# Optimization experiments

Measured on AMD Instinct MI355X. Metric: run time of the kernel, lower is better.

Reference implementation:

```python
import jax, jax.numpy as jnp
import numpy as np

B, LQ, LK, E, HID, H = 4, 1024, 2048, 512, 512, 8


def _ln(x, g, b, eps=1e-5):
    mu = jnp.mean(x, -1, keepdims=True)
    var = jnp.mean((x - mu) ** 2, -1, keepdims=True)
    return (x - mu) * jax.lax.rsqrt(var + eps) * g + b


def _mha(q_in, k_in, v_in, Wq, bq, Wk, bk, Wv, bv, Wo, bo, nheads, q_valid, k_valid):
    # torch nn.MultiheadAttention (batch_first, eval/dropout=0) math
    Bq, Lq, Em = q_in.shape
    Lk = k_in.shape[1]
    hd = Em // nheads
    q = (q_in @ Wq.T + bq).reshape(Bq, Lq, nheads, hd)
    k = (k_in @ Wk.T + bk).reshape(Bq, Lk, nheads, hd)
    v = (v_in @ Wv.T + bv).reshape(Bq, Lk, nheads, hd)
    scale = 1.0 / np.sqrt(hd).astype(np.float32)
    s = jnp.einsum('bqhd,bkhd->bhqk', q, k) * scale
    if k_valid is not None:
        # valid query rows may only attend to valid key columns
        s = jnp.where(k_valid[:, None, None, :], s, jnp.finfo(s.dtype).min)
    w = jax.nn.softmax(s, axis=-1)
    # rows beyond a sample's length are fully masked in the torch nested path
    # (softmax -> NaN, later nan_to_num'd to 0); we zero them directly.
    w = jnp.where(q_valid[:, None, :, None], w, 0.0)
    o = jnp.einsum('bhqk,bkhd->bqhd', w, v).reshape(Bq, Lq, Em)
    return o @ Wo.T + bo, jnp.mean(w, axis=1)  # weights averaged over heads


def setup_inputs() -> dict:
    key = jax.random.key(0)
    ks = jax.random.split(key, 32)
    p = lambda i, shape: 0.02 * jax.random.normal(ks[i], shape, dtype=jnp.float32)
    inp = {
        'queries': jax.random.normal(ks[0], (B, LQ, E), dtype=jnp.float32),
        'keys': jax.random.normal(ks[1], (B, LK, E), dtype=jnp.float32),
        'q_len': jax.random.randint(ks[2], (B,), 1, LQ + 1),
        # cross-attention params
        'cWq': p(3, (E, E)), 'cbq': jnp.zeros((E,)),
        'cWk': p(4, (E, E)), 'cbk': jnp.zeros((E,)),
        'cWv': p(5, (E, E)), 'cbv': jnp.zeros((E,)),
        'cWo': p(6, (E, E)), 'cbo': jnp.zeros((E,)),
        # self-attention params
        'sWq': p(7, (HID, HID)), 'sbq': jnp.zeros((HID,)),
        'sWk': p(8, (HID, HID)), 'sbk': jnp.zeros((HID,)),
        'sWv': p(9, (HID, HID)), 'sbv': jnp.zeros((HID,)),
        'sWo': p(10, (HID, HID)), 'sbo': jnp.zeros((HID,)),
        # ffn + norms
        'Wf': p(11, (HID, E)), 'bf': jnp.zeros((HID,)),
        'g_cross': jnp.ones((E,)), 'b_cross': jnp.zeros((E,)),
        'g_ffn': jnp.ones((HID,)), 'b_ffn': jnp.zeros((HID,)),
        'g_self': jnp.ones((HID,)), 'b_self': jnp.zeros((HID,)),
    }
    return inp


def reference(queries, keys, q_len,
              cWq, cbq, cWk, cbk, cWv, cbv, cWo, cbo,
              sWq, sbq, sWk, sbk, sWv, sbv, sWo, sbo,
              Wf, bf, g_cross, b_cross, g_ffn, b_ffn, g_self, b_self):
    valid = jnp.arange(LQ)[None, :] < q_len[:, None]  # [B, LQ] ragged lengths
    q = jnp.where(valid[..., None], queries, 0.0)     # nested -> padded with 0
    # cross attention: valid rows attend to ALL keys (per the nested mask)
    cross, weights = _mha(q, keys, keys, cWq, cbq, cWk, cbk, cWv, cbv, cWo, cbo,
                          H, valid, None)
    q = _ln(jax.nn.silu(cross + q), g_cross, b_cross)
    f = q @ Wf.T + bf
    q = _ln(jax.nn.silu(q + f), g_ffn, b_ffn)  # q_dim == hidden_dim branch
    q = jnp.where(valid[..., None], q, 0.0)    # torch.nan_to_num on padded rows
    # self attention: valid rows attend only to valid rows of the same sample
    so, _ = _mha(q, q, q, sWq, sbq, sWk, sbk, sWv, sbv, sWo, sbo, H, valid, valid)
    q = _ln(jax.nn.silu(q + so), g_self, b_self)
    q = jnp.where(valid[..., None], q, 0.0)    # padded rows discarded by unbind
    return q, weights
```

## Files before the change

kernel.cpp:

```cpp
#include <hip/hip_runtime.h>

#define BB 4
#define SLQ 1024
#define SLK 2048
#define EE 512
#define HH 8
#define HD 64

typedef unsigned short u16;
typedef __attribute__((ext_vector_type(8))) short s16x8;
typedef __attribute__((ext_vector_type(4))) float f32x4;

__device__ __forceinline__ float bf2f(u16 u) {
  union { unsigned int i; float f; } v; v.i = ((unsigned int)u) << 16; return v.f;
}
__device__ __forceinline__ u16 f2bf(float f) {
  union { float f; unsigned int i; } v; v.f = f;
  unsigned int i = v.i;
  return (u16)((i + 0x7fffu + ((i >> 16) & 1u)) >> 16);
}

__device__ __forceinline__ void async16(const u16* g, u16* l) {
  __builtin_amdgcn_global_load_lds(
      (const __attribute__((address_space(1))) unsigned int*)g,
      (__attribute__((address_space(3))) unsigned int*)l, 16, 0, 0);
}

template<int BM, int BN, int MODE, int SKIPQ>
__global__ __launch_bounds__(256, (BM == 128 ? 4 : 6))
void gemm_nt(const u16* __restrict__ A, const u16* __restrict__ Bm,
             const float* __restrict__ bias, u16* __restrict__ C,
             int M, int N, int K, int lda, int ldb, int ldc,
             long sAz, long sBz, long sCz, float alpha, int Lsub,
             const int* __restrict__ qlen)
{
  constexpr int WTM = BM / 2, WTN = BN / 2;
  constexpr int MI = WTM / 16, NI = WTN / 16;
  constexpr int EPAD = WTN + 8;
  constexpr int SM1 = (BM + BN) * 32;
  constexpr int SM2 = (MODE == 0) ? 4 * WTM * EPAD : 0;
  constexpr int SM = (SM1 > SM2) ? SM1 : SM2;

  const int z = blockIdx.z;
  const int tileM = blockIdx.y * BM;
  const int tileN = blockIdx.x * BN;

  if (SKIPQ == 1) { if (tileM >= qlen[z >> 3]) return; }
  if (SKIPQ == 2) { int b = tileM >> 10; if ((tileM & 1023) >= qlen[b]) return; }

  __shared__ __align__(16) u16 smem[SM];
  u16* ldsA = smem;
  u16* ldsB = smem + BM * 32;

  const int t = threadIdx.x;
  const int lane = t & 63;
  const int wave = t >> 6;
  const int waveM = wave >> 1;
  const int waveN = wave & 1;
  const int lm = lane & 15;
  const int kg = lane >> 4;

  const u16* Ab = A + (long)z * sAz + (long)tileM * lda;
  const u16* Bb = Bm + (long)z * sBz + (long)tileN * ldb;

  f32x4 acc[MI][NI];
#pragma unroll
  for (int i = 0; i < MI; ++i)
#pragma unroll
    for (int j = 0; j < NI; ++j) acc[i][j] = (f32x4){0.f, 0.f, 0.f, 0.f};

  for (int kt = 0; kt < K; kt += 32) {
    __syncthreads();
#pragma unroll
    for (int i = 0; i < (BM * 4) / 256; ++i) {
      int c = i * 256 + t;
      async16(Ab + (long)(c >> 2) * lda + kt + (c & 3) * 8, ldsA + (c - lane) * 8);
    }
#pragma unroll
    for (int i = 0; i < (BN * 4) / 256; ++i) {
      int c = i * 256 + t;
      async16(Bb + (long)(c >> 2) * ldb + kt + (c & 3) * 8, ldsB + (c - lane) * 8);
    }
    __syncthreads();

    s16x8 aF[MI], bF[NI];
#pragma unroll
    for (int i = 0; i < MI; ++i)
      aF[i] = *(const s16x8*)&ldsA[(waveM * WTM + i * 16 + lm) * 32 + kg * 8];
#pragma unroll
    for (int j = 0; j < NI; ++j)
      bF[j] = *(const s16x8*)&ldsB[(waveN * WTN + j * 16 + lm) * 32 + kg * 8];
#pragma unroll
    for (int i = 0; i < MI; ++i)
#pragma unroll
      for (int j = 0; j < NI; ++j)
        acc[i][j] = __builtin_amdgcn_mfma_f32_16x16x32_bf16(aF[i], bF[j], acc[i][j], 0, 0, 0);
  }

  if (MODE == 0) {
    u16* ep = smem + wave * (WTM * EPAD);
    __syncthreads();
#pragma unroll
    for (int i = 0; i < MI; ++i)
#pragma unroll
      for (int j = 0; j < NI; ++j) {
        int n = waveN * WTN + j * 16 + lm;
        float bv = bias ? bias[tileN + n] : 0.0f;
#pragma unroll
        for (int r = 0; r < 4; ++r)
          ep[(i * 16 + kg * 4 + r) * EPAD + j * 16 + lm] = f2bf(acc[i][j][r] * alpha + bv);
      }
    const long Crow = (long)z * sCz + (long)(tileM + waveM * WTM) * ldc + tileN + waveN * WTN;
#pragma unroll
    for (int it = 0; it < (WTM * WTN) / 512; ++it) {
      int idx = it * 64 + lane;
      int row = idx / (WTN / 8), seg = idx % (WTN / 8);
      *(uint4*)&C[Crow + (long)row * ldc + seg * 8] =
          *(const uint4*)&ep[row * EPAD + seg * 8];
    }
  } else {
#pragma unroll
    for (int j = 0; j < NI; ++j) {
      int n = tileN + waveN * WTN + j * 16 + lm;
      float bv = bias ? bias[n] : 0.0f;
#pragma unroll
      for (int i = 0; i < MI; ++i) {
#pragma unroll
        for (int r = 0; r < 4; ++r) {
          int m = tileM + waveM * WTM + i * 16 + kg * 4 + r;
          float v = acc[i][j][r] * alpha + bv;
          int b = m / Lsub, l = m - b * Lsub;
          int h = n >> 6, d = n & 63;
          C[(((long)(b * HH + h) * Lsub + l) << 6) + d] = f2bf(v);
        }
      }
    }
  }
}

template<int BM, int BN, int SKIPQ, int NPROJ>
__global__ __launch_bounds__(256, 6)
void gemm_proj(const u16* __restrict__ A,
               const u16* B0, const u16* B1, const u16* B2,
               const float* bias0, const float* bias1, const float* bias2,
               u16* C0, u16* C1, u16* C2,
               int M, int lda, int Lsub, const int* __restrict__ qlen)
{
  constexpr int WTM = BM / 2, WTN = BN / 2;
  constexpr int MI = WTM / 16, NI = WTN / 16;

  const int z = blockIdx.z;
  const int tileM = blockIdx.y * BM;
  const int tileN = blockIdx.x * BN;
  if (SKIPQ == 2) { int b = tileM >> 10; if ((tileM & 1023) >= qlen[b]) return; }

  const u16* Bm = (z == 0) ? B0 : (z == 1) ? B1 : B2;
  const float* bias = (z == 0) ? bias0 : (z == 1) ? bias1 : bias2;
  u16* C = (z == 0) ? C0 : (z == 1) ? C1 : C2;
  const bool tr = (z == NPROJ - 1);

  __shared__ __align__(16) u16 smem[(BM + BN) * 32];
  u16* ldsA = smem;
  u16* ldsB = smem + BM * 32;

  const int t = threadIdx.x;
  const int lane = t & 63;
  const int wave = t >> 6;
  const int waveM = wave >> 1;
  const int waveN = wave & 1;
  const int lm = lane & 15;
  const int kg = lane >> 4;

  const u16* Ab = A + (long)tileM * lda;
  const u16* Bb = Bm + (long)tileN * EE;

  f32x4 acc[MI][NI];
#pragma unroll
  for (int i = 0; i < MI; ++i)
#pragma unroll
    for (int j = 0; j < NI; ++j) acc[i][j] = (f32x4){0.f, 0.f, 0.f, 0.f};

  for (int kt = 0; kt < EE; kt += 32) {
    __syncthreads();
#pragma unroll
    for (int i = 0; i < (BM * 4) / 256; ++i) {
      int c = i * 256 + t;
      async16(Ab + (long)(c >> 2) * lda + kt + (c & 3) * 8, ldsA + (c - lane) * 8);
    }
#pragma unroll
    for (int i = 0; i < (BN * 4) / 256; ++i) {
      int c = i * 256 + t;
      async16(Bb + (long)(c >> 2) * EE + kt + (c & 3) * 8, ldsB + (c - lane) * 8);
    }
    __syncthreads();

    s16x8 aF[MI], bF[NI];
#pragma unroll
    for (int i = 0; i < MI; ++i)
      aF[i] = *(const s16x8*)&ldsA[(waveM * WTM + i * 16 + lm) * 32 + kg * 8];
#pragma unroll
    for (int j = 0; j < NI; ++j)
      bF[j] = *(const s16x8*)&ldsB[(waveN * WTN + j * 16 + lm) * 32 + kg * 8];
#pragma unroll
    for (int i = 0; i < MI; ++i)
#pragma unroll
      for (int j = 0; j < NI; ++j)
        acc[i][j] = __builtin_amdgcn_mfma_f32_16x16x32_bf16(aF[i], bF[j], acc[i][j], 0, 0, 0);
  }

  if (!tr) {
#pragma unroll
    for (int j = 0; j < NI; ++j) {
      int n = tileN + waveN * WTN + j * 16 + lm;
      float bv = bias[n];
#pragma unroll
      for (int i = 0; i < MI; ++i)
#pragma unroll
        for (int r = 0; r < 4; ++r) {
          int m = tileM + waveM * WTM + i * 16 + kg * 4 + r;
          int b = m / Lsub, l = m - b * Lsub;
          int h = n >> 6, d = n & 63;
          C[(((long)(b * HH + h) * Lsub + l) << 6) + d] = f2bf(acc[i][j][r] + bv);
        }
    }
  } else {
    constexpr int PAD = BM + 8;
    const int bb = tileM / Lsub;
    const int l0 = tileM - bb * Lsub;
#pragma unroll
    for (int c = 0; c < BN / 32; ++c) {
      __syncthreads();
#pragma unroll
      for (int j = 0; j < NI; ++j) {
        int nloc = waveN * WTN + j * 16 + lm;
        if (nloc >= c * 32 && nloc < c * 32 + 32) {
          int nl = nloc - c * 32;
          float bv = bias[tileN + nloc];
#pragma unroll
          for (int i = 0; i < MI; ++i)
#pragma unroll
            for (int r = 0; r < 4; ++r) {
              int mm = waveM * WTM + i * 16 + kg * 4 + r;
              smem[nl * PAD + mm] = f2bf(acc[i][j][r] + bv);
            }
        }
      }
      __syncthreads();
#pragma unroll
      for (int v = 0; v < (32 * BM) / (256 * 8); ++v) {
        int idx = v * 256 + t;
        int nl = idx / (BM / 8), m8 = idx % (BM / 8);
        int n = tileN + c * 32 + nl;
        int h = n >> 6, d = n & 63;
        *(uint4*)&C[((long)(bb * HH + h) * HD + d) * Lsub + l0 + m8 * 8] =
            *(const uint4*)&smem[nl * PAD + m8 * 8];
      }
    }
  }
}

__global__ __launch_bounds__(256)
void softmax_stats_wmean(const u16* __restrict__ S, float* __restrict__ outw,
                         float2* __restrict__ stats, const int* __restrict__ qlen) {
  int row = blockIdx.x;
  int b = row >> 10, q = row & 1023;
  int t = threadIdx.x, lane = t & 63, w = t >> 6;
  float* wr = outw + (long)row * SLK;
  if (q >= qlen[b]) {
    float4 z = {0.f, 0.f, 0.f, 0.f};
    *(float4*)(wr + t * 8) = z; *(float4*)(wr + t * 8 + 4) = z;
    return;
  }
  __shared__ float acc4[4][2048];
#pragma unroll
  for (int hh = 0; hh < 2; ++hh) {
    int h = 2 * w + hh;
    const u16* p = S + ((long)((b * HH + h) * SLQ + q)) * SLK;
    float x[4][8];
    float m = -1e30f;
#pragma unroll
    for (int c = 0; c < 4; ++c) {
      s16x8 v = *(const s16x8*)(p + c * 512 + lane * 8);
#pragma unroll
      for (int j = 0; j < 8; ++j) { x[c][j] = bf2f((u16)v[j]); m = fmaxf(m, x[c][j]); }
    }
#pragma unroll
    for (int o = 1; o <= 32; o <<= 1) m = fmaxf(m, __shfl_xor(m, o));
    float s = 0.f;
#pragma unroll
    for (int c = 0; c < 4; ++c)
#pragma unroll
      for (int j = 0; j < 8; ++j) { x[c][j] = __expf(x[c][j] - m); s += x[c][j]; }
#pragma unroll
    for (int o = 1; o <= 32; o <<= 1) s += __shfl_xor(s, o);
    if (lane == 0) stats[(long)(b * HH + h) * SLQ + q] = (float2){m, s};
    float sc = 0.125f / s;
#pragma unroll
    for (int c = 0; c < 4; ++c) {
      float4 v0 = {x[c][0] * sc, x[c][1] * sc, x[c][2] * sc, x[c][3] * sc};
      float4 v1 = {x[c][4] * sc, x[c][5] * sc, x[c][6] * sc, x[c][7] * sc};
      if (hh == 0) {
        *(float4*)&acc4[w][c * 512 + lane * 8] = v0;
        *(float4*)&acc4[w][c * 512 + lane * 8 + 4] = v1;
      } else {
        float4 a0 = *(const float4*)&acc4[w][c * 512 + lane * 8];
        float4 a1 = *(const float4*)&acc4[w][c * 512 + lane * 8 + 4];
        a0.x += v0.x; a0.y += v0.y; a0.z += v0.z; a0.w += v0.w;
        a1.x += v1.x; a1.y += v1.y; a1.z += v1.z; a1.w += v1.w;
        *(float4*)&acc4[w][c * 512 + lane * 8] = a0;
        *(float4*)&acc4[w][c * 512 + lane * 8 + 4] = a1;
      }
    }
  }
  __syncthreads();
#pragma unroll
  for (int u = 0; u < 2; ++u) {
    int k = t * 8 + u * 4;
    float4 s0 = *(const float4*)&acc4[0][k];
    float4 s1 = *(const float4*)&acc4[1][k];
    float4 s2 = *(const float4*)&acc4[2][k];
    float4 s3 = *(const float4*)&acc4[3][k];
    float4 o = {s0.x + s1.x + s2.x + s3.x, s0.y + s1.y + s2.y + s3.y,
                s0.z + s1.z + s2.z + s3.z, s0.w + s1.w + s2.w + s3.w};
    *(float4*)(wr + k) = o;
  }
}

__global__ __launch_bounds__(256, 6)
void pv_cross(const u16* __restrict__ S, const u16* __restrict__ Vt,
              const float2* __restrict__ stats, u16* __restrict__ Opart,
              const int* __restrict__ qlen)
{
  const int qt = blockIdx.x;
  const int bh = blockIdx.y;
  const int kc = blockIdx.z;
  const int b = bh >> 3;
  if (qt * 64 >= qlen[b]) return;

  __shared__ __align__(16) u16 Vl[64 * 136];

  const int t = threadIdx.x, lane = t & 63, w = t >> 6;
  const int lm = lane & 15, quad = lane >> 4;

  const int qrow = qt * 64 + w * 16 + lm;
  const u16* Sb = S + ((long)bh * SLQ + qrow) * SLK;
  const u16* Vb = Vt + (long)bh * HD * SLK;
  const float mrow = stats[(long)bh * SLQ + qrow].x;

  f32x4 O[4];
#pragma unroll
  for (int n = 0; n < 4; ++n) O[n] = (f32x4){0.f, 0.f, 0.f, 0.f};

  for (int ks = 0; ks < 4; ++ks) {
    const int k0 = kc * 512 + ks * 128;
    __syncthreads();
    for (int c = t; c < 1024; c += 256) {
      int d = c >> 4, c16 = c & 15;
      *(uint4*)&Vl[d * 136 + c16 * 8] = *(const uint4*)(Vb + (long)d * SLK + k0 + c16 * 8);
    }
    __syncthreads();
#pragma unroll
    for (int kk = 0; kk < 4; ++kk) {
      s16x8 raw = *(const s16x8*)(Sb + k0 + kk * 32 + quad * 8);
      s16x8 aP;
#pragma unroll
      for (int j = 0; j < 8; ++j)
        aP[j] = (short)f2bf(__expf(bf2f((u16)raw[j]) - mrow));
#pragma unroll
      for (int n = 0; n < 4; ++n) {
        s16x8 bV = *(const s16x8*)&Vl[(n * 16 + lm) * 136 + kk * 32 + quad * 8];
        O[n] = __builtin_amdgcn_mfma_f32_16x16x32_bf16(aP, bV, O[n], 0, 0, 0);
      }
    }
  }

#pragma unroll
  for (int r = 0; r < 4; ++r) {
    int qr2 = qt * 64 + w * 16 + quad * 4 + r;
#pragma unroll
    for (int n = 0; n < 4; ++n)
      Opart[(((long)bh * SLQ + qr2) * 4 + kc) * 64 + n * 16 + lm] = f2bf(O[n][r]);
  }
}

__global__ __launch_bounds__(256)
void pv_combine_cross(const u16* __restrict__ Opart, const float2* __restrict__ stats,
                      u16* __restrict__ attn, const int* __restrict__ qlen)
{
  int gr = blockIdx.x * 16 + (threadIdx.x >> 4);
  int bh = gr >> 10, q = gr & 1023;
  int b = bh >> 3, h = bh & 7;
  if (q >= qlen[b]) return;
  int d = (threadIdx.x & 15) * 4;
  float ax = 0.f, ay = 0.f, az = 0.f, aw = 0.f;
#pragma unroll
  for (int c = 0; c < 4; ++c) {
    const u16* p = Opart + ((long)gr * 4 + c) * 64 + d;
    ax += bf2f(p[0]); ay += bf2f(p[1]); az += bf2f(p[2]); aw += bf2f(p[3]);
  }
  float inv = 1.0f / stats[gr].y;
  unsigned int lo = (unsigned int)f2bf(ax * inv) | ((unsigned int)f2bf(ay * inv) << 16);
  unsigned int hi = (unsigned int)f2bf(az * inv) | ((unsigned int)f2bf(aw * inv) << 16);
  *(uint2*)&attn[((long)b * SLQ + q) * EE + h * HD + d] = (uint2){lo, hi};
}

__global__ __launch_bounds__(256, 3)
void self_flash_chunk(const u16* __restrict__ Qc, const u16* __restrict__ Kc,
                      const u16* __restrict__ Vt, u16* __restrict__ Opart,
                      float2* __restrict__ ml, const int* __restrict__ qlen)
{
  const int qt = blockIdx.x;
  const int bh = blockIdx.y;
  const int ck = blockIdx.z;
  const int b = bh >> 3;
  const int kmax = qlen[b];
  if (qt * 64 >= kmax || ck * 256 >= kmax) return;

  __shared__ __align__(16) u16 Kt[128 * 72];
  __shared__ __align__(16) u16 Vl[64 * 136];
  __shared__ __align__(16) u16 Pl[4 * 16 * 136];

  const int t = threadIdx.x, lane = t & 63, w = t >> 6;
  const int col = lane & 15, quad = lane >> 4;

  const u16* Qb = Qc + (long)bh * SLQ * HD;
  const u16* Kb = Kc + (long)bh * SLQ * HD;
  const u16* Vb = Vt + (long)bh * HD * SLQ;

  s16x8 aQ[2];
#pragma unroll
  for (int kk = 0; kk < 2; ++kk)
    aQ[kk] = *(const s16x8*)(Qb + (long)(qt * 64 + w * 16 + col) * HD + kk * 32 + quad * 8);

  f32x4 O[4];
  float mr[4], lr[4];
#pragma unroll
  for (int n = 0; n < 4; ++n) O[n] = (f32x4){0.f, 0.f, 0.f, 0.f};
#pragma unroll
  for (int r = 0; r < 4; ++r) { mr[r] = -1e30f; lr[r] = 0.f; }

  u16* Pw = Pl + w * 16 * 136;

  for (int kt = 0; kt < 2; ++kt) {
    const int k0 = ck * 256 + kt * 128;
    if (k0 >= kmax) break;
    __syncthreads();
    for (int c = t; c < 1024; c += 256) {
      int r = c >> 3, c8 = c & 7;
      *(uint4*)&Kt[r * 72 + c8 * 8] = *(const uint4*)(Kb + (long)(k0 + r) * HD + c8 * 8);
    }
    for (int c = t; c < 1024; c += 256) {
      int d = c >> 4, c16 = c & 15;
      *(uint4*)&Vl[d * 136 + c16 * 8] = *(const uint4*)(Vb + (long)d * SLQ + k0 + c16 * 8);
    }
    __syncthreads();

    f32x4 s[8];
#pragma unroll
    for (int j = 0; j < 8; ++j) s[j] = (f32x4){0.f, 0.f, 0.f, 0.f};
#pragma unroll
    for (int j = 0; j < 8; ++j)
#pragma unroll
      for (int kk = 0; kk < 2; ++kk) {
        s16x8 bK = *(const s16x8*)&Kt[(j * 16 + col) * 72 + kk * 32 + quad * 8];
        s[j] = __builtin_amdgcn_mfma_f32_16x16x32_bf16(aQ[kk], bK, s[j], 0, 0, 0);
      }
#pragma unroll
    for (int j = 0; j < 8; ++j) {
      bool ok = (k0 + j * 16 + col) < kmax;
#pragma unroll
      for (int r = 0; r < 4; ++r)
        s[j][r] = ok ? s[j][r] * 0.125f : -1e30f;
    }
#pragma unroll
    for (int r = 0; r < 4; ++r) {
      float tm = s[0][r];
#pragma unroll
      for (int j = 1; j < 8; ++j) tm = fmaxf(tm, s[j][r]);
#pragma unroll
      for (int o = 1; o <= 8; o <<= 1) tm = fmaxf(tm, __shfl_xor(tm, o));
      float mnew = fmaxf(mr[r], tm);
      float alpha = __expf(mr[r] - mnew);
      mr[r] = mnew;
      float ps = 0.f;
#pragma unroll
      for (int j = 0; j < 8; ++j) {
        float p = __expf(s[j][r] - mnew);
        s[j][r] = p;
        ps += p;
      }
#pragma unroll
      for (int o = 1; o <= 8; o <<= 1) ps += __shfl_xor(ps, o);
      lr[r] = lr[r] * alpha + ps;
#pragma unroll
      for (int n = 0; n < 4; ++n) O[n][r] *= alpha;
    }
#pragma unroll
    for (int j = 0; j < 8; ++j)
#pragma unroll
      for (int r = 0; r < 4; ++r)
        Pw[(quad * 4 + r) * 136 + j * 16 + col] = f2bf(s[j][r]);
#pragma unroll
    for (int kk = 0; kk < 4; ++kk) {
      s16x8 aP = *(const s16x8*)&Pw[col * 136 + kk * 32 + quad * 8];
#pragma unroll
      for (int n = 0; n < 4; ++n) {
        s16x8 bV = *(const s16x8*)&Vl[(n * 16 + col) * 136 + kk * 32 + quad * 8];
        O[n] = __builtin_amdgcn_mfma_f32_16x16x32_bf16(aP, bV, O[n], 0, 0, 0);
      }
    }
  }

#pragma unroll
  for (int r = 0; r < 4; ++r) {
    int q = qt * 64 + w * 16 + quad * 4 + r;
    long gq = (long)bh * SLQ + q;
#pragma unroll
    for (int n = 0; n < 4; ++n)
      Opart[(gq * 4 + ck) * 64 + n * 16 + col] = f2bf(O[n][r]);
    if (col == 0) ml[gq * 4 + ck] = (float2){mr[r], lr[r]};
  }
}

__global__ __launch_bounds__(256)
void self_combine(const u16* __restrict__ Opart, const float2* __restrict__ ml,
                  u16* __restrict__ attn, const int* __restrict__ qlen)
{
  int gr = blockIdx.x * 16 + (threadIdx.x >> 4);
  int bh = gr >> 10, q = gr & 1023;
  int b = bh >> 3, h = bh & 7;
  int kmax = qlen[b];
  if (q >= kmax) return;
  int NC = (kmax + 255) >> 8;
  int d = (threadIdx.x & 15) * 4;
  long base = (long)gr * 4;
  float M = -1e30f;
  for (int c = 0; c < NC; ++c) M = fmaxf(M, ml[base + c].x);
  float L = 0.f;
  float ax = 0.f, ay = 0.f, az = 0.f, aw = 0.f;
  for (int c = 0; c < NC; ++c) {
    float2 st = ml[base + c];
    float wgt = __expf(st.x - M);
    L += st.y * wgt;
    const u16* p = Opart + (base + c) * 64 + d;
    ax += bf2f(p[0]) * wgt; ay += bf2f(p[1]) * wgt;
    az += bf2f(p[2]) * wgt; aw += bf2f(p[3]) * wgt;
  }
  float inv = 1.0f / L;
  unsigned int lo = (unsigned int)f2bf(ax * inv) | ((unsigned int)f2bf(ay * inv) << 16);
  unsigned int hi = (unsigned int)f2bf(az * inv) | ((unsigned int)f2bf(aw * inv) << 16);
  *(uint2*)&attn[((long)b * SLQ + q) * EE + h * HD + d] = (uint2){lo, hi};
}

__global__ __launch_bounds__(256)
void cvt_all(const float* __restrict__ queries, const float* __restrict__ keys,
             const int* __restrict__ qlen,
             const float* w0, const float* w1, const float* w2, const float* w3,
             const float* w4, const float* w5, const float* w6, const float* w7,
             const float* w8,
             u16* __restrict__ q0, u16* __restrict__ keysb, u16* __restrict__ Wb) {
  int blk = blockIdx.x;
  int t = threadIdx.x;
  const float* src;
  u16* dst;
  long off;
  bool mask = false;
  int b = 0, q = 0;
  if (blk < 1024) {
    off = (long)blk * 2048 + t * 8;
    int row = (int)(off >> 9);
    b = row >> 10; q = row & 1023;
    mask = true;
    src = queries; dst = q0;
  } else if (blk < 3072) {
    off = (long)(blk - 1024) * 2048 + t * 8;
    src = keys; dst = keysb;
  } else {
    int mat = (blk - 3072) >> 7, part = (blk - 3072) & 127;
    const float* srcs[9] = {w0, w1, w2, w3, w4, w5, w6, w7, w8};
    src = srcs[mat];
    off = (long)part * 2048 + t * 8;
    dst = Wb + (long)mat * EE * EE;
  }
  s16x8 o = (s16x8){0, 0, 0, 0, 0, 0, 0, 0};
  if (!mask || q < qlen[b]) {
    float4 a = *(const float4*)&src[off];
    float4 c = *(const float4*)&src[off + 4];
    o[0] = (short)f2bf(a.x); o[1] = (short)f2bf(a.y);
    o[2] = (short)f2bf(a.z); o[3] = (short)f2bf(a.w);
    o[4] = (short)f2bf(c.x); o[5] = (short)f2bf(c.y);
    o[6] = (short)f2bf(c.z); o[7] = (short)f2bf(c.w);
  }
  *(s16x8*)&dst[off] = o;
}

__device__ __forceinline__ float blockSum(float v, float* red4) {
#pragma unroll
  for (int o = 32; o; o >>= 1) v += __shfl_xor(v, o);
  if ((threadIdx.x & 63) == 0) red4[threadIdx.x >> 6] = v;
  __syncthreads();
  v = red4[0] + red4[1] + red4[2] + red4[3];
  __syncthreads();
  return v;
}

template<int OUTF32>
__global__ __launch_bounds__(256)
void silu_ln_kernel(const u16* __restrict__ x1, const u16* __restrict__ x2,
                    const float* __restrict__ g, const float* __restrict__ beta,
                    const int* __restrict__ qlen, void* __restrict__ outv, int mode) {
  int row = blockIdx.x;
  int b = row >> 10, q = row & 1023;
  int t = threadIdx.x;
  if (mode && q >= qlen[b]) {
    if (mode == 1) {
      if (OUTF32) {
        float* o = (float*)outv + (long)row * EE;
        o[2 * t] = 0.f; o[2 * t + 1] = 0.f;
      } else {
        u16* o = (u16*)outv + (long)row * EE;
        *(unsigned int*)&o[2 * t] = 0u;
      }
    }
    return;
  }
  __shared__ float red4[4];
  const u16* p1 = x1 + (long)row * EE;
  const u16* p2 = x2 + (long)row * EE;
  float a0 = bf2f(p1[2 * t]) + bf2f(p2[2 * t]);
  float a1 = bf2f(p1[2 * t + 1]) + bf2f(p2[2 * t + 1]);
  a0 = a0 / (1.f + __expf(-a0));
  a1 = a1 / (1.f + __expf(-a1));
  float mu = blockSum(a0 + a1, red4) * (1.f / 512.f);
  float d0 = a0 - mu, d1 = a1 - mu;
  float var = blockSum(d0 * d0 + d1 * d1, red4) * (1.f / 512.f);
  float rs = rsqrtf(var + 1e-5f);
  float r0 = d0 * rs * g[2 * t] + beta[2 * t];
  float r1 = d1 * rs * g[2 * t + 1] + beta[2 * t + 1];
  if (OUTF32) {
    float* o = (float*)outv + (long)row * EE;
    o[2 * t] = r0; o[2 * t + 1] = r1;
  } else {
    u16* o = (u16*)outv + (long)row * EE;
    o[2 * t] = f2bf(r0); o[2 * t + 1] = f2bf(r1);
  }
}

extern "C" void kernel_launch(void* const* d_in, const int* in_sizes, int n_in,
                              void* d_out, int out_size, void* d_ws, size_t ws_size,
                              hipStream_t stream) {
  const float* queries = (const float*)d_in[0];
  const float* keys    = (const float*)d_in[1];
  const int*   qlen    = (const int*)d_in[2];
  const float* cWq = (const float*)d_in[3],  *cbq = (const float*)d_in[4];
  const float* cWk = (const float*)d_in[5],  *cbk = (const float*)d_in[6];
  const float* cWv = (const float*)d_in[7],  *cbv = (const float*)d_in[8];
  const float* cWo = (const float*)d_in[9],  *cbo = (const float*)d_in[10];
  const float* sWq = (const float*)d_in[11], *sbq = (const float*)d_in[12];
  const float* sWk = (const float*)d_in[13], *sbk = (const float*)d_in[14];
  const float* sWv = (const float*)d_in[15], *sbv = (const float*)d_in[16];
  const float* sWo = (const float*)d_in[17], *sbo = (const float*)d_in[18];
  const float* Wf  = (const float*)d_in[19], *bfb = (const float*)d_in[20];
  const float* g_cross = (const float*)d_in[21], *b_cross = (const float*)d_in[22];
  const float* g_ffn   = (const float*)d_in[23], *b_ffn   = (const float*)d_in[24];
  const float* g_self  = (const float*)d_in[25], *b_self  = (const float*)d_in[26];

  float* out_q = (float*)d_out;
  float* out_w = out_q + (long)BB * SLQ * EE;

  u16* ws = (u16*)d_ws;
  u16* S     = ws;
  u16* Qc    = S   + (long)BB * HH * SLQ * SLK;
  u16* Kc    = Qc  + (long)BB * HH * SLQ * HD;
  u16* Vt    = Kc  + (long)BB * HH * SLK * HD;
  u16* q0    = Vt  + (long)BB * HH * SLK * HD;
  u16* keysb = q0  + (long)BB * SLQ * EE;
  u16* attn  = keysb + (long)BB * SLK * EE;
  u16* proj  = attn + (long)BB * SLQ * EE;
  u16* q1    = proj + (long)BB * SLQ * EE;
  u16* fbuf  = q1  + (long)BB * SLQ * EE;
  u16* q2    = fbuf + (long)BB * SLQ * EE;
  u16* Wb    = q2  + (long)BB * SLQ * EE;
  const long WSLOT = (long)EE * EE;
  u16*    Cpb  = Wb + 9 * WSLOT;
  float2* stat = (float2*)(Cpb + 8388608);

  u16*    OpS = S;
  float2* mlS = (float2*)(S + 8388608);

  u16* bWq = Wb + 0 * WSLOT; u16* bWk = Wb + 1 * WSLOT; u16* bWv = Wb + 2 * WSLOT;
  u16* bWo = Wb + 3 * WSLOT; u16* bsWq = Wb + 4 * WSLOT; u16* bsWk = Wb + 5 * WSLOT;
  u16* bsWv = Wb + 6 * WSLOT; u16* bsWo = Wb + 7 * WSLOT; u16* bWf = Wb + 8 * WSLOT;

  dim3 blk(256);
  const int MQ = BB * SLQ;
  const int MK = BB * SLK;

  cvt_all<<<dim3(3072 + 9 * 128), blk, 0, stream>>>(
      queries, keys, qlen, cWq, cWk, cWv, cWo, sWq, sWk, sWv, sWo, Wf, q0, keysb, Wb);

  gemm_nt<64, 64, 1, 2><<<dim3(EE / 64, MQ / 64, 1), blk, 0, stream>>>(
      q0, bWq, cbq, Qc, MQ, EE, EE, EE, EE, 0, 0, 0, 0, 1.0f, SLQ, qlen);
  gemm_proj<64, 64, 0, 2><<<dim3(EE / 64, MK / 64, 2), blk, 0, stream>>>(
      keysb, bWk, bWv, nullptr, cbk, cbv, nullptr, Kc, Vt, nullptr, MK, EE, SLK, qlen);

  gemm_nt<128, 128, 0, 1><<<dim3(SLK / 128, SLQ / 128, BB * HH), blk, 0, stream>>>(
      Qc, Kc, nullptr, S, SLQ, SLK, HD, HD, HD, SLK,
      (long)SLQ * HD, (long)SLK * HD, (long)SLQ * SLK, 0.125f, 0, qlen);

  softmax_stats_wmean<<<dim3(BB * SLQ), blk, 0, stream>>>(S, out_w, stat, qlen);

  pv_cross<<<dim3(16, 32, 4), blk, 0, stream>>>(S, Vt, stat, Cpb, qlen);
  pv_combine_cross<<<dim3(2048), blk, 0, stream>>>(Cpb, stat, attn, qlen);

  gemm_nt<64, 64, 0, 2><<<dim3(EE / 64, MQ / 64, 1), blk, 0, stream>>>(
      attn, bWo, cbo, proj, MQ, EE, EE, EE, EE, EE, 0, 0, 0, 1.0f, SLQ, qlen);

  silu_ln_kernel<0><<<dim3(MQ), blk, 0, stream>>>(proj, q0, g_cross, b_cross, qlen, q1, 2);

  gemm_nt<64, 64, 0, 2><<<dim3(EE / 64, MQ / 64, 1), blk, 0, stream>>>(
      q1, bWf, bfb, fbuf, MQ, EE, EE, EE, EE, EE, 0, 0, 0, 1.0f, SLQ, qlen);

  silu_ln_kernel<0><<<dim3(MQ), blk, 0, stream>>>(q1, fbuf, g_ffn, b_ffn, qlen, q2, 1);

  gemm_proj<64, 64, 2, 3><<<dim3(EE / 64, MQ / 64, 3), blk, 0, stream>>>(
      q2, bsWq, bsWk, bsWv, sbq, sbk, sbv, Qc, Kc, Vt, MQ, EE, SLQ, qlen);

  self_flash_chunk<<<dim3(16, 32, 4), blk, 0, stream>>>(Qc, Kc, Vt, OpS, mlS, qlen);
  self_combine<<<dim3(2048), blk, 0, stream>>>(OpS, mlS, attn, qlen);

  gemm_nt<64, 64, 0, 2><<<dim3(EE / 64, MQ / 64, 1), blk, 0, stream>>>(
      attn, bsWo, sbo, proj, MQ, EE, EE, EE, EE, EE, 0, 0, 0, 1.0f, SLQ, qlen);

  silu_ln_kernel<1><<<dim3(MQ), blk, 0, stream>>>(q2, proj, g_self, b_self, qlen, out_q, 1);
}
```

Measured before the change: 318.3 us.

## Replace materialized cross-attention scores with flash chunks and recomputed head-mean weights

The cross-attention path no longer writes the full bf16 score matrix S to global memory. A split-K flash-style kernel with online softmax computes partial outputs, and a combine kernel merges them and produces the row max and sum stats. A separate kernel then recomputes QK^T per head to build the head-averaged weight output. This removes the large S write and its repeated reads, at the cost of computing QK^T twice.

Result: slower. 378.7 us (+19.0%).

```diff
diff --git a/kernel.cpp b/kernel.cpp
--- a/kernel.cpp
+++ b/kernel.cpp
@@ -259,116 +259,104 @@
   }
 }
 
-__global__ __launch_bounds__(256)
-void softmax_stats_wmean(const u16* __restrict__ S, float* __restrict__ outw,
-                         float2* __restrict__ stats, const int* __restrict__ qlen) {
-  int row = blockIdx.x;
-  int b = row >> 10, q = row & 1023;
-  int t = threadIdx.x, lane = t & 63, w = t >> 6;
-  float* wr = outw + (long)row * SLK;
-  if (q >= qlen[b]) {
-    float4 z = {0.f, 0.f, 0.f, 0.f};
-    *(float4*)(wr + t * 8) = z; *(float4*)(wr + t * 8 + 4) = z;
-    return;
-  }
-  __shared__ float acc4[4][2048];
-#pragma unroll
-  for (int hh = 0; hh < 2; ++hh) {
-    int h = 2 * w + hh;
-    const u16* p = S + ((long)((b * HH + h) * SLQ + q)) * SLK;
-    float x[4][8];
-    float m = -1e30f;
-#pragma unroll
-    for (int c = 0; c < 4; ++c) {
-      s16x8 v = *(const s16x8*)(p + c * 512 + lane * 8);
-#pragma unroll
-      for (int j = 0; j < 8; ++j) { x[c][j] = bf2f((u16)v[j]); m = fmaxf(m, x[c][j]); }
-    }
-#pragma unroll
-    for (int o = 1; o <= 32; o <<= 1) m = fmaxf(m, __shfl_xor(m, o));
-    float s = 0.f;
-#pragma unroll
-    for (int c = 0; c < 4; ++c)
-#pragma unroll
-      for (int j = 0; j < 8; ++j) { x[c][j] = __expf(x[c][j] - m); s += x[c][j]; }
-#pragma unroll
-    for (int o = 1; o <= 32; o <<= 1) s += __shfl_xor(s, o);
-    if (lane == 0) stats[(long)(b * HH + h) * SLQ + q] = (float2){m, s};
-    float sc = 0.125f / s;
-#pragma unroll
-    for (int c = 0; c < 4; ++c) {
-      float4 v0 = {x[c][0] * sc, x[c][1] * sc, x[c][2] * sc, x[c][3] * sc};
-      float4 v1 = {x[c][4] * sc, x[c][5] * sc, x[c][6] * sc, x[c][7] * sc};
-      if (hh == 0) {
-        *(float4*)&acc4[w][c * 512 + lane * 8] = v0;
-        *(float4*)&acc4[w][c * 512 + lane * 8 + 4] = v1;
-      } else {
-        float4 a0 = *(const float4*)&acc4[w][c * 512 + lane * 8];
-        float4 a1 = *(const float4*)&acc4[w][c * 512 + lane * 8 + 4];
-        a0.x += v0.x; a0.y += v0.y; a0.z += v0.z; a0.w += v0.w;
-        a1.x += v1.x; a1.y += v1.y; a1.z += v1.z; a1.w += v1.w;
-        *(float4*)&acc4[w][c * 512 + lane * 8] = a0;
-        *(float4*)&acc4[w][c * 512 + lane * 8 + 4] = a1;
-      }
-    }
-  }
-  __syncthreads();
-#pragma unroll
-  for (int u = 0; u < 2; ++u) {
-    int k = t * 8 + u * 4;
-    float4 s0 = *(const float4*)&acc4[0][k];
-    float4 s1 = *(const float4*)&acc4[1][k];
-    float4 s2 = *(const float4*)&acc4[2][k];
-    float4 s3 = *(const float4*)&acc4[3][k];
-    float4 o = {s0.x + s1.x + s2.x + s3.x, s0.y + s1.y + s2.y + s3.y,
-                s0.z + s1.z + s2.z + s3.z, s0.w + s1.w + s2.w + s3.w};
-    *(float4*)(wr + k) = o;
-  }
-}
-
-__global__ __launch_bounds__(256, 6)
-void pv_cross(const u16* __restrict__ S, const u16* __restrict__ Vt,
-              const float2* __restrict__ stats, u16* __restrict__ Opart,
-              const int* __restrict__ qlen)
+__global__ __launch_bounds__(256, 3)
+void cross_flash_chunk(const u16* __restrict__ Qc, const u16* __restrict__ Kc,
+                       const u16* __restrict__ Vt, u16* __restrict__ Opart,
+                       float2* __restrict__ ml, const int* __restrict__ qlen)
 {
   const int qt = blockIdx.x;
   const int bh = blockIdx.y;
-  const int kc = blockIdx.z;
+  const int ck = blockIdx.z;
   const int b = bh >> 3;
   if (qt * 64 >= qlen[b]) return;
 
+  __shared__ __align__(16) u16 Kt[128 * 72];
   __shared__ __align__(16) u16 Vl[64 * 136];
+  __shared__ __align__(16) u16 Pl[4 * 16 * 136];
 
   const int t = threadIdx.x, lane = t & 63, w = t >> 6;
-  const int lm = lane & 15, quad = lane >> 4;
-
-  const int qrow = qt * 64 + w * 16 + lm;
-  const u16* Sb = S + ((long)bh * SLQ + qrow) * SLK;
+  const int col = lane & 15, quad = lane >> 4;
+
+  const u16* Qb = Qc + (long)bh * SLQ * HD;
+  const u16* Kb = Kc + (long)bh * SLK * HD;
   const u16* Vb = Vt + (long)bh * HD * SLK;
-  const float mrow = stats[(long)bh * SLQ + qrow].x;
+
+  s16x8 aQ[2];
+#pragma unroll
+  for (int kk = 0; kk < 2; ++kk)
+    aQ[kk] = *(const s16x8*)(Qb + (long)(qt * 64 + w * 16 + col) * HD + kk * 32 + quad * 8);
 
   f32x4 O[4];
+  float mr[4], lr[4];
 #pragma unroll
   for (int n = 0; n < 4; ++n) O[n] = (f32x4){0.f, 0.f, 0.f, 0.f};
-
-  for (int ks = 0; ks < 4; ++ks) {
-    const int k0 = kc * 512 + ks * 128;
+#pragma unroll
+  for (int r = 0; r < 4; ++r) { mr[r] = -1e30f; lr[r] = 0.f; }
+
+  u16* Pw = Pl + w * 16 * 136;
+
+  for (int kt = 0; kt < 4; ++kt) {
+    const int k0 = ck * 512 + kt * 128;
     __syncthreads();
+    for (int c = t; c < 1024; c += 256) {
+      int r = c >> 3, c8 = c & 7;
+      *(uint4*)&Kt[r * 72 + c8 * 8] = *(const uint4*)(Kb + (long)(k0 + r) * HD + c8 * 8);
+    }
     for (int c = t; c < 1024; c += 256) {
       int d = c >> 4, c16 = c & 15;
       *(uint4*)&Vl[d * 136 + c16 * 8] = *(const uint4*)(Vb + (long)d * SLK + k0 + c16 * 8);
     }
     __syncthreads();
+
+    f32x4 s[8];
+#pragma unroll
+    for (int j = 0; j < 8; ++j) s[j] = (f32x4){0.f, 0.f, 0.f, 0.f};
+#pragma unroll
+    for (int j = 0; j < 8; ++j)
+#pragma unroll
+      for (int kk = 0; kk < 2; ++kk) {
+        s16x8 bK = *(const s16x8*)&Kt[(j * 16 + col) * 72 + kk * 32 + quad * 8];
+        s[j] = __builtin_amdgcn_mfma_f32_16x16x32_bf16(aQ[kk], bK, s[j], 0, 0, 0);
+      }
+#pragma unroll
+    for (int j = 0; j < 8; ++j)
+#pragma unroll
+      for (int r = 0; r < 4; ++r)
+        s[j][r] *= 0.125f;
+#pragma unroll
+    for (int r = 0; r < 4; ++r) {
+      float tm = s[0][r];
+#pragma unroll
+      for (int j = 1; j < 8; ++j) tm = fmaxf(tm, s[j][r]);
+#pragma unroll
+      for (int o = 1; o <= 8; o <<= 1) tm = fmaxf(tm, __shfl_xor(tm, o));
+      float mnew = fmaxf(mr[r], tm);
+      float alpha = __expf(mr[r] - mnew);
+      mr[r] = mnew;
+      float ps = 0.f;
+#pragma unroll
+      for (int j = 0; j < 8; ++j) {
+        float p = __expf(s[j][r] - mnew);
+        s[j][r] = p;
+        ps += p;
+      }
+#pragma unroll
+      for (int o = 1; o <= 8; o <<= 1) ps += __shfl_xor(ps, o);
+      lr[r] = lr[r] * alpha + ps;
+#pragma unroll
+      for (int n = 0; n < 4; ++n) O[n][r] *= alpha;
+    }
+#pragma unroll
+    for (int j = 0; j < 8; ++j)
+#pragma unroll
+      for (int r = 0; r < 4; ++r)
+        Pw[(quad * 4 + r) * 136 + j * 16 + col] = f2bf(s[j][r]);
 #pragma unroll
     for (int kk = 0; kk < 4; ++kk) {
-      s16x8 raw = *(const s16x8*)(Sb + k0 + kk * 32 + quad * 8);
-      s16x8 aP;
-#pragma unroll
-      for (int j = 0; j < 8; ++j)
-        aP[j] = (short)f2bf(__expf(bf2f((u16)raw[j]) - mrow));
+      s16x8 aP = *(const s16x8*)&Pw[col * 136 + kk * 32 + quad * 8];
 #pragma unroll
       for (int n = 0; n < 4; ++n) {
-        s16x8 bV = *(const s16x8*)&Vl[(n * 16 + lm) * 136 + kk * 32 + quad * 8];
+        s16x8 bV = *(const s16x8*)&Vl[(n * 16 + col) * 136 + kk * 32 + quad * 8];
         O[n] = __builtin_amdgcn_mfma_f32_16x16x32_bf16(aP, bV, O[n], 0, 0, 0);
       }
     }
@@ -376,32 +364,111 @@
 
 #pragma unroll
   for (int r = 0; r < 4; ++r) {
-    int qr2 = qt * 64 + w * 16 + quad * 4 + r;
+    int q = qt * 64 + w * 16 + quad * 4 + r;
+    long gq = (long)bh * SLQ + q;
 #pragma unroll
     for (int n = 0; n < 4; ++n)
-      Opart[(((long)bh * SLQ + qr2) * 4 + kc) * 64 + n * 16 + lm] = f2bf(O[n][r]);
+      Opart[(gq * 4 + ck) * 64 + n * 16 + col] = f2bf(O[n][r]);
+    if (col == 0) ml[gq * 4 + ck] = (float2){mr[r], lr[r]};
   }
 }
 
 __global__ __launch_bounds__(256)
-void pv_combine_cross(const u16* __restrict__ Opart, const float2* __restrict__ stats,
-                      u16* __restrict__ attn, const int* __restrict__ qlen)
+void cross_combine(const u16* __restrict__ Opart, const float2* __restrict__ ml,
+                   u16* __restrict__ attn, float2* __restrict__ stat,
+                   const int* __restrict__ qlen)
 {
   int gr = blockIdx.x * 16 + (threadIdx.x >> 4);
   int bh = gr >> 10, q = gr & 1023;
   int b = bh >> 3, h = bh & 7;
   if (q >= qlen[b]) return;
   int d = (threadIdx.x & 15) * 4;
+  long base = (long)gr * 4;
+  float M = -1e30f;
+#pragma unroll
+  for (int c = 0; c < 4; ++c) M = fmaxf(M, ml[base + c].x);
+  float L = 0.f;
   float ax = 0.f, ay = 0.f, az = 0.f, aw = 0.f;
 #pragma unroll
   for (int c = 0; c < 4; ++c) {
-    const u16* p = Opart + ((long)gr * 4 + c) * 64 + d;
-    ax += bf2f(p[0]); ay += bf2f(p[1]); az += bf2f(p[2]); aw += bf2f(p[3]);
-  }
-  float inv = 1.0f / stats[gr].y;
+    float2 st = ml[base + c];
+    float wgt = __expf(st.x - M);
+    L += st.y * wgt;
+    const u16* p = Opart + (base + c) * 64 + d;
+    ax += bf2f(p[0]) * wgt; ay += bf2f(p[1]) * wgt;
+    az += bf2f(p[2]) * wgt; aw += bf2f(p[3]) * wgt;
+  }
+  if (d == 0) stat[gr] = (float2){M, L};
+  float inv = 1.0f / L;
   unsigned int lo = (unsigned int)f2bf(ax * inv) | ((unsigned int)f2bf(ay * inv) << 16);
   unsigned int hi = (unsigned int)f2bf(az * inv) | ((unsigned int)f2bf(aw * inv) << 16);
   *(uint2*)&attn[((long)b * SLQ + q) * EE + h * HD + d] = (uint2){lo, hi};
+}
+
+__global__ __launch_bounds__(256, 4)
+void wmean_recompute(const u16* __restrict__ Qc, const u16* __restrict__ Kc,
+                     const float2* __restrict__ stat, float* __restrict__ outw,
+                     const int* __restrict__ qlen)
+{
+  const int kq = blockIdx.x;
+  const int qg = blockIdx.y;
+  const int b  = blockIdx.z;
+  const int q0 = qg * 16;
+  const int t = threadIdx.x, lane = t & 63, w = t >> 6;
+  const int col = lane & 15, quad = lane >> 4;
+  const int qn = qlen[b];
+  float* wr = outw + ((long)b * SLQ + q0) * SLK + kq * 512;
+
+  if (q0 >= qn) {
+    float4 z = {0.f, 0.f, 0.f, 0.f};
+    for (int i = t; i < 16 * 128; i += 256) {
+      int row = i >> 7, c = (i & 127) * 4;
+      *(float4*)&wr[(long)row * SLK + c] = z;
+    }
+    return;
+  }
+
+  const int kbase = kq * 512 + w * 128;
+  f32x4 acc[8];
+#pragma unroll
+  for (int j = 0; j < 8; ++j) acc[j] = (f32x4){0.f, 0.f, 0.f, 0.f};
+
+#pragma unroll 1
+  for (int h = 0; h < 8; ++h) {
+    const int bh = b * 8 + h;
+    const u16* Qb = Qc + ((long)bh * SLQ + q0) * HD;
+    const u16* Kb = Kc + (long)bh * SLK * HD;
+    s16x8 aQ0 = *(const s16x8*)(Qb + col * HD + quad * 8);
+    s16x8 aQ1 = *(const s16x8*)(Qb + col * HD + 32 + quad * 8);
+    float m_[4], il_[4];
+#pragma unroll
+    for (int r = 0; r < 4; ++r) {
+      float2 st = stat[(long)bh * SLQ + q0 + quad * 4 + r];
+      m_[r] = st.x; il_[r] = 0.125f / st.y;
+    }
+#pragma unroll
+    for (int j = 0; j < 8; ++j) {
+      int k0 = kbase + j * 16;
+      const u16* Kp = Kb + (long)(k0 + col) * HD;
+      s16x8 bK0 = *(const s16x8*)(Kp + quad * 8);
+      s16x8 bK1 = *(const s16x8*)(Kp + 32 + quad * 8);
+      f32x4 s = (f32x4){0.f, 0.f, 0.f, 0.f};
+      s = __builtin_amdgcn_mfma_f32_16x16x32_bf16(aQ0, bK0, s, 0, 0, 0);
+      s = __builtin_amdgcn_mfma_f32_16x16x32_bf16(aQ1, bK1, s, 0, 0, 0);
+#pragma unroll
+      for (int r = 0; r < 4; ++r)
+        acc[j][r] += __expf(s[r] * 0.125f - m_[r]) * il_[r];
+    }
+  }
+
+#pragma unroll
+  for (int r = 0; r < 4; ++r) {
+    int row = quad * 4 + r;
+    bool v = (q0 + row) < qn;
+#pragma unroll
+    for (int j = 0; j < 8; ++j)
+      wr[(long)row * SLK + w * 128 + j * 16 + col] = v ? acc[j][r] : 0.f;
+  }
 }
 
 __global__ __launch_bounds__(256, 3)
@@ -685,6 +752,8 @@
   u16*    Cpb  = Wb + 9 * WSLOT;
   float2* stat = (float2*)(Cpb + 8388608);
 
+  float2* mlC = (float2*)(S + 33554432);
+
   u16*    OpS = S;
   float2* mlS = (float2*)(S + 8388608);
 
@@ -704,14 +773,9 @@
   gemm_proj<64, 64, 0, 2><<<dim3(EE / 64, MK / 64, 2), blk, 0, stream>>>(
       keysb, bWk, bWv, nullptr, cbk, cbv, nullptr, Kc, Vt, nullptr, MK, EE, SLK, qlen);
 
-  gemm_nt<128, 128, 0, 1><<<dim3(SLK / 128, SLQ / 128, BB * HH), blk, 0, stream>>>(
-      Qc, Kc, nullptr, S, SLQ, SLK, HD, HD, HD, SLK,
-      (long)SLQ * HD, (long)SLK * HD, (long)SLQ * SLK, 0.125f, 0, qlen);
-
-  softmax_stats_wmean<<<dim3(BB * SLQ), blk, 0, stream>>>(S, out_w, stat, qlen);
-
-  pv_cross<<<dim3(16, 32, 4), blk, 0, stream>>>(S, Vt, stat, Cpb, qlen);
-  pv_combine_cross<<<dim3(2048), blk, 0, stream>>>(Cpb, stat, attn, qlen);
+  cross_flash_chunk<<<dim3(16, 32, 4), blk, 0, stream>>>(Qc, Kc, Vt, Cpb, mlC, qlen);
+  cross_combine<<<dim3(2048), blk, 0, stream>>>(Cpb, mlC, attn, stat, qlen);
+  wmean_recompute<<<dim3(4, 64, BB), blk, 0, stream>>>(Qc, Kc, stat, out_w, qlen);
 
   gemm_nt<64, 64, 0, 2><<<dim3(EE / 64, MQ / 64, 1), blk, 0, stream>>>(
       attn, bWo, cbo, proj, MQ, EE, EE, EE, EE, EE, 0, 0, 0, 1.0f, SLQ, qlen);
```
